# Optimization experiments

Measured on AMD Instinct MI355X. Metric: run time of the kernel, lower is better.

## Reference

```python
import jax, jax.numpy as jnp
import numpy as np

N = 100000   # nodes
E = 1600000  # edges (avg degree 16)
D = 64       # in_channels
OUT = 64     # out_channels


def setup_inputs() -> dict:
    key = jax.random.key(0)
    k1, k2, k3, k4, k5 = jax.random.split(key, 5)
    x = jax.random.normal(k1, (N, D), jnp.float32)
    edge_index = jax.random.randint(k2, (2, E), 0, N, dtype=jnp.int32)
    x0 = jax.random.normal(k3, (N, D), jnp.float32)
    W_weight = jax.random.normal(k4, (OUT, D), jnp.float32) * (1.0 / np.sqrt(D))
    W_bias = jax.random.normal(k5, (OUT,), jnp.float32) * 0.01
    return {"x": x, "edge_index": edge_index, "x0": x0,
            "W_weight": W_weight, "W_bias": W_bias}


def reference(x, edge_index, x0, W_bias, W_weight):
    n = x.shape[0]
    # gcn_norm with add_self_loops=True (PyG default), improved=False
    self_loops = jnp.arange(n, dtype=edge_index.dtype)
    row = jnp.concatenate([edge_index[0], self_loops])  # source nodes
    col = jnp.concatenate([edge_index[1], self_loops])  # target nodes
    w = jnp.ones(row.shape[0], dtype=x.dtype)
    deg = jax.ops.segment_sum(w, col, num_segments=n)   # in-degree (+1 self loop)
    deg_inv_sqrt = jnp.where(deg > 0, jax.lax.rsqrt(jnp.maximum(deg, 1e-12)), 0.0)
    norm = deg_inv_sqrt[row] * deg_inv_sqrt[col]        # [E+N]
    # SpMM: adj_t = SparseTensor(row=col, col=row) -> out[c] = sum_e norm_e * x[row_e]
    agg = jax.ops.segment_sum(x[row] * norm[:, None], col, num_segments=n)  # [N, D]
    # use_init=False, use_weight=True -> trailing Linear
    return agg @ W_weight.T + W_bias
```

## Files before the change

kernel.cpp:

```cpp
#include <hip/hip_runtime.h>


#define NBMAX 400
#define CAP   5120

typedef short bf16x8 __attribute__((ext_vector_type(8)));
typedef float f32x4  __attribute__((ext_vector_type(4)));

__device__ inline float bflo(unsigned u) { return __uint_as_float(u << 16); }
__device__ inline float bfhi(unsigned u) { return __uint_as_float(u & 0xFFFF0000u); }
__device__ inline unsigned short f2bf(float f) {
    unsigned u = __float_as_uint(f);
    u += 0x7FFFu + ((u >> 16) & 1u);
    return (unsigned short)(u >> 16);
}

__global__ void k_initcur(int* __restrict__ gcur, int NB) {
    int b = threadIdx.x;
    if (b < NB) gcur[b] = b * CAP;
}

__global__ __launch_bounds__(256) void k_bin(const int* __restrict__ row,
                                             const int* __restrict__ col,
                                             int* __restrict__ gcur,
                                             unsigned int* __restrict__ ebuf, int E) {
    __shared__ unsigned int   sorted4[4096];
    __shared__ unsigned short sbkt[4096];
    __shared__ int h[NBMAX], hstart[NBMAX], hcur[NBMAX], gof[NBMAX];
    int t = threadIdx.x;
    int base = blockIdx.x * 4096;
    int total = min(4096, E - base);

    int rr[16], cc[16];
    #pragma unroll
    for (int i = 0; i < 4; ++i) {
        int e0 = (t + i * 256) * 4;
        if (e0 + 3 < total) {
            int4 r4 = *(const int4*)(row + base + e0);
            int4 c4 = *(const int4*)(col + base + e0);
            rr[i*4+0]=r4.x; rr[i*4+1]=r4.y; rr[i*4+2]=r4.z; rr[i*4+3]=r4.w;
            cc[i*4+0]=c4.x; cc[i*4+1]=c4.y; cc[i*4+2]=c4.z; cc[i*4+3]=c4.w;
        } else {
            #pragma unroll
            for (int j = 0; j < 4; ++j) {
                int e = e0 + j;
                if (e < total) { rr[i*4+j] = row[base+e]; cc[i*4+j] = col[base+e]; }
                else cc[i*4+j] = -1;
            }
        }
    }
    for (int b = t; b < NBMAX; b += 256) h[b] = 0;
    __syncthreads();
    #pragma unroll
    for (int i = 0; i < 16; ++i)
        if (cc[i] >= 0) atomicAdd(&h[cc[i] >> 8], 1);
    __syncthreads();
    if (t < 64) {
        int lo = t * 7;
        int loc[7]; int s = 0;
        #pragma unroll
        for (int i = 0; i < 7; ++i) {
            loc[i] = s;
            int idx = lo + i;
            s += (idx < NBMAX) ? h[idx] : 0;
        }
        int incl = s;
        for (int off = 1; off < 64; off <<= 1) {
            int v = __shfl_up(incl, off);
            if (t >= off) incl += v;
        }
        int ex = incl - s;
        #pragma unroll
        for (int i = 0; i < 7; ++i) {
            int idx = lo + i;
            if (idx < NBMAX) hstart[idx] = ex + loc[i];
        }
    }
    __syncthreads();
    for (int b = t; b < NBMAX; b += 256) hcur[b] = hstart[b];
    __syncthreads();
    #pragma unroll
    for (int i = 0; i < 16; ++i) {
        if (cc[i] >= 0) {
            int b = cc[i] >> 8;
            int rank = atomicAdd(&hcur[b], 1);
            sorted4[rank] = (unsigned)rr[i] | ((unsigned)(cc[i] & 255) << 24);
            sbkt[rank] = (unsigned short)b;
        }
    }
    for (int b = t; b < NBMAX; b += 256) {
        int m = h[b];
        gof[b] = m ? atomicAdd(&gcur[b], m) : 0;
    }
    __syncthreads();
    for (int i = t; i < total; i += 256) {
        int b = sbkt[i];
        ebuf[gof[b] + (i - hstart[b])] = sorted4[i];
    }
}

__global__ __launch_bounds__(256) void k_cnt(const unsigned int* __restrict__ ebuf,
                                             const int* __restrict__ gcur,
                                             float* __restrict__ dinv, int n) {
    __shared__ int h[256];
    int b = blockIdx.x, t = threadIdx.x;
    int s0 = b * CAP;
    int count = min(gcur[b] - s0, CAP);
    h[t] = 0;
    __syncthreads();
    for (int i = t; i < count; i += 256) atomicAdd(&h[ebuf[s0 + i] >> 24], 1);
    __syncthreads();
    int c = b * 256 + t;
    if (c < n) dinv[c] = rsqrtf((float)(h[t] + 1));
}

__global__ __launch_bounds__(256) void k_gemm(const float* __restrict__ x,
                                              const float* __restrict__ W,
                                              const float* __restrict__ dinv,
                                              unsigned short* __restrict__ yb, int n) {
    __shared__ __align__(16) unsigned short xs[64][72];
    __shared__ __align__(16) unsigned short Wb[64][72];
    int t = threadIdx.x;
    long long total = (long long)n * 64;
    long long xbase = (long long)blockIdx.x * 4096;
    #pragma unroll
    for (int i = 0; i < 4; ++i) {
        int idx = t + i * 256;
        int r = idx >> 4, c4 = (idx & 15) << 2;
        long long g = xbase + (long long)idx * 4;
        float4 v;
        if (g + 3 < total) v = *(const float4*)(x + g);
        else {
            v.x = (g + 0 < total) ? x[g + 0] : 0.f;
            v.y = (g + 1 < total) ? x[g + 1] : 0.f;
            v.z = (g + 2 < total) ? x[g + 2] : 0.f;
            v.w = (g + 3 < total) ? x[g + 3] : 0.f;
        }
        ushort4 o; o.x = f2bf(v.x); o.y = f2bf(v.y); o.z = f2bf(v.z); o.w = f2bf(v.w);
        *(ushort4*)&xs[r][c4] = o;
        float4 wv = *(const float4*)(W + idx * 4);
        ushort4 wo; wo.x = f2bf(wv.x); wo.y = f2bf(wv.y); wo.z = f2bf(wv.z); wo.w = f2bf(wv.w);
        *(ushort4*)&Wb[r][c4] = wo;
    }
    __syncthreads();
    int lane = t & 63, wid = t >> 6;
    int m  = wid * 16 + (lane & 15);
    int kg = (lane >> 4) * 8;
    bf16x8 a0 = *(bf16x8*)&xs[m][kg];
    bf16x8 a1 = *(bf16x8*)&xs[m][32 + kg];
    int bn = lane & 15;
    f32x4 acc0 = {0.f,0.f,0.f,0.f}, acc1 = acc0, acc2 = acc0, acc3 = acc0;
    {
        bf16x8 b0 = *(bf16x8*)&Wb[bn][kg], b1 = *(bf16x8*)&Wb[bn][32 + kg];
        acc0 = __builtin_amdgcn_mfma_f32_16x16x32_bf16(a0, b0, acc0, 0, 0, 0);
        acc0 = __builtin_amdgcn_mfma_f32_16x16x32_bf16(a1, b1, acc0, 0, 0, 0);
    }
    {
        bf16x8 b0 = *(bf16x8*)&Wb[bn + 16][kg], b1 = *(bf16x8*)&Wb[bn + 16][32 + kg];
        acc1 = __builtin_amdgcn_mfma_f32_16x16x32_bf16(a0, b0, acc1, 0, 0, 0);
        acc1 = __builtin_amdgcn_mfma_f32_16x16x32_bf16(a1, b1, acc1, 0, 0, 0);
    }
    {
        bf16x8 b0 = *(bf16x8*)&Wb[bn + 32][kg], b1 = *(bf16x8*)&Wb[bn + 32][32 + kg];
        acc2 = __builtin_amdgcn_mfma_f32_16x16x32_bf16(a0, b0, acc2, 0, 0, 0);
        acc2 = __builtin_amdgcn_mfma_f32_16x16x32_bf16(a1, b1, acc2, 0, 0, 0);
    }
    {
        bf16x8 b0 = *(bf16x8*)&Wb[bn + 48][kg], b1 = *(bf16x8*)&Wb[bn + 48][32 + kg];
        acc3 = __builtin_amdgcn_mfma_f32_16x16x32_bf16(a0, b0, acc3, 0, 0, 0);
        acc3 = __builtin_amdgcn_mfma_f32_16x16x32_bf16(a1, b1, acc3, 0, 0, 0);
    }
    int rbase = blockIdx.x * 64 + wid * 16 + (lane >> 4) * 4;
    #pragma unroll
    for (int i = 0; i < 4; ++i) {
        int r = rbase + i;
        if (r < n) {
            float dv = dinv[r];
            long long ro = (long long)r * 64 + (lane & 15);
            yb[ro +  0] = f2bf(dv * acc0[i]);
            yb[ro + 16] = f2bf(dv * acc1[i]);
            yb[ro + 32] = f2bf(dv * acc2[i]);
            yb[ro + 48] = f2bf(dv * acc3[i]);
        }
    }
}

__global__ __launch_bounds__(1024) void k_aggr(const unsigned int* __restrict__ ebuf,
                                               const int* __restrict__ gcur,
                                               const float* __restrict__ dinv,
                                               const unsigned short* __restrict__ yb,
                                               const float* __restrict__ bias,
                                               float* __restrict__ out, int n) {
    __shared__ int h[256], hstart[256], hc[256], wsum[4];
    __shared__ int sbuf[CAP];
    int b = blockIdx.x, t = threadIdx.x;
    int s0 = b * CAP;
    int count = min(gcur[b] - s0, CAP);

    if (t < 256) h[t] = 0;
    __syncthreads();
    unsigned rec[5];
    #pragma unroll
    for (int k = 0; k < 5; ++k) {
        int i = t + k * 1024;
        if (i < count) {
            unsigned p = ebuf[s0 + i];
            rec[k] = p;
            atomicAdd(&h[p >> 24], 1);
        }
    }
    __syncthreads();
    if (t < 256) {
        int v = h[t];
        int lane = t & 63, wid = t >> 6;
        int incl = v;
        #pragma unroll
        for (int off = 1; off < 64; off <<= 1) {
            int u = __shfl_up(incl, off);
            if (lane >= off) incl += u;
        }
        hstart[t] = incl;
        if (lane == 63) wsum[wid] = incl;
    }
    __syncthreads();
    if (t < 256) {
        int wid = t >> 6;
        int add = 0;
        for (int w = 0; w < wid; ++w) add += wsum[w];
        int ex = hstart[t] - h[t] + add;
        hstart[t] = ex;
        hc[t] = ex;
    }
    __syncthreads();
    #pragma unroll
    for (int k = 0; k < 5; ++k) {
        int i = t + k * 1024;
        if (i < count) {
            unsigned p = rec[k];
            int r = atomicAdd(&hc[p >> 24], 1);
            sbuf[r] = (int)(p & 0x1FFFFu);
        }
    }
    __syncthreads();

    int lane = t & 63, w = t >> 6;
    int g = lane >> 4, q = lane & 15;
    #pragma unroll
    for (int r = 0; r < 4; ++r) {
        int cl = r * 64 + w * 4 + g;
        int c = b * 256 + cl;
        if (c >= n) continue;
        int start = hstart[cl], len = h[cl];
        float a0 = 0.f, a1 = 0.f, a2 = 0.f, a3 = 0.f;
        if (len > 0) {
            int sc = sbuf[start];
            for (int i = 0; i < len; ++i) {
                int sn = (i + 1 < len) ? sbuf[start + i + 1] : 0;
                float2 v = *(const float2*)(yb + (long long)sc * 64 + (q << 2));
                unsigned u0 = __float_as_uint(v.x), u1 = __float_as_uint(v.y);
                a0 += bflo(u0); a1 += bfhi(u0);
                a2 += bflo(u1); a3 += bfhi(u1);
                sc = sn;
            }
        }
        {
            float2 v = *(const float2*)(yb + (long long)c * 64 + (q << 2));
            unsigned u0 = __float_as_uint(v.x), u1 = __float_as_uint(v.y);
            a0 += bflo(u0); a1 += bfhi(u0);
            a2 += bflo(u1); a3 += bfhi(u1);
        }
        float dc = dinv[c];
        float4 bv = *(const float4*)(bias + (q << 2));
        *(float4*)(out + (long long)c * 64 + (q << 2)) =
            make_float4(dc * a0 + bv.x, dc * a1 + bv.y,
                        dc * a2 + bv.z, dc * a3 + bv.w);
    }
}

extern "C" void kernel_launch(void* const* d_in, const int* in_sizes, int n_in,
                              void* d_out, int out_size, void* d_ws, size_t ws_size,
                              hipStream_t stream) {
    const float* x    = (const float*)d_in[0];
    const int*   ei   = (const int*)d_in[1];
    const float* W    = (const float*)d_in[3];
    const float* bias = (const float*)d_in[4];
    float* out = (float*)d_out;

    int n = in_sizes[0] / 64;
    int E = in_sizes[1] / 2;
    const int* row = ei;
    const int* col = ei + E;

    int NB = (n + 255) / 256;

    char* ws = (char*)d_ws;
    size_t off = 0;
    auto alloc = [&](size_t bytes) { char* p = ws + off; off += (bytes + 15) & ~size_t(15); return p; };
    int*            gcur = (int*)  alloc((size_t)NB * 4);
    float*          dinv = (float*)alloc((size_t)n * 4);
    unsigned short* yb   = (unsigned short*)alloc((size_t)n * 64 * 2);
    unsigned int*   ebuf = (unsigned int*)alloc((size_t)NB * CAP * 4);

    int nbE = (E + 4095) / 4096;

    k_initcur<<<1, 512, 0, stream>>>(gcur, NB);
    k_bin <<<nbE, 256, 0, stream>>>(row, col, gcur, ebuf, E);
    k_cnt <<<NB, 256, 0, stream>>>(ebuf, gcur, dinv, n);
    k_gemm<<<(n + 63) / 64, 256, 0, stream>>>(x, W, dinv, yb, n);
    k_aggr<<<NB, 1024, 0, stream>>>(ebuf, gcur, dinv, yb, bias, out, n);
}
```

Baseline: 178.1 us.

## Balance aggregation by degree-ranked node pairing and widen gathers to 8 lanes per node

```diff
diff --git a/kernel.cpp b/kernel.cpp
--- a/kernel.cpp
+++ b/kernel.cpp
@@ -13,6 +13,13 @@
     unsigned u = __float_as_uint(f);
     u += 0x7FFFu + ((u >> 16) & 1u);
     return (unsigned short)(u >> 16);
+}
+
+__device__ inline void acc8(float* a, float4 v) {
+    unsigned x = __float_as_uint(v.x), y = __float_as_uint(v.y);
+    unsigned z = __float_as_uint(v.z), w = __float_as_uint(v.w);
+    a[0] += bflo(x); a[1] += bfhi(x); a[2] += bflo(y); a[3] += bfhi(y);
+    a[4] += bflo(z); a[5] += bfhi(z); a[6] += bflo(w); a[7] += bfhi(w);
 }
 
 __global__ void k_initcur(int* __restrict__ gcur, int NB) {
@@ -192,12 +199,13 @@
                                                const float* __restrict__ bias,
                                                float* __restrict__ out, int n) {
     __shared__ int h[256], hstart[256], hc[256], wsum[4];
+    __shared__ int rnk[256], slotmap[256];
     __shared__ int sbuf[CAP];
     int b = blockIdx.x, t = threadIdx.x;
     int s0 = b * CAP;
     int count = min(gcur[b] - s0, CAP);
 
-    if (t < 256) h[t] = 0;
+    if (t < 256) { h[t] = 0; rnk[t] = 0; }
     __syncthreads();
     unsigned rec[5];
     #pragma unroll
@@ -222,6 +230,17 @@
         hstart[t] = incl;
         if (lane == 63) wsum[wid] = incl;
     }
+    {
+        int cl2 = t & 255, part = t >> 8;
+        int lt = h[cl2];
+        int base2 = part << 6;
+        int rk = 0;
+        for (int u2 = base2; u2 < base2 + 64; ++u2) {
+            int lu = h[u2];
+            rk += ((lu > lt) || (lu == lt && u2 < cl2)) ? 1 : 0;
+        }
+        if (rk) atomicAdd(&rnk[cl2], rk);
+    }
     __syncthreads();
     if (t < 256) {
         int wid = t >> 6;
@@ -230,6 +249,7 @@
         int ex = hstart[t] - h[t] + add;
         hstart[t] = ex;
         hc[t] = ex;
+        slotmap[rnk[t]] = t;
     }
     __syncthreads();
     #pragma unroll
@@ -244,36 +264,49 @@
     __syncthreads();
 
     int lane = t & 63, w = t >> 6;
-    int g = lane >> 4, q = lane & 15;
-    #pragma unroll
-    for (int r = 0; r < 4; ++r) {
-        int cl = r * 64 + w * 4 + g;
+    int g = lane >> 3, q = lane & 7;
+    int qo = q << 3;
+    #pragma unroll 1
+    for (int r = 0; r < 2; ++r) {
+        int slot = w * 8 + g;
+        int cl = slotmap[r == 0 ? slot : 255 - slot];
         int c = b * 256 + cl;
         if (c >= n) continue;
         int start = hstart[cl], len = h[cl];
-        float a0 = 0.f, a1 = 0.f, a2 = 0.f, a3 = 0.f;
-        if (len > 0) {
-            int sc = sbuf[start];
-            for (int i = 0; i < len; ++i) {
-                int sn = (i + 1 < len) ? sbuf[start + i + 1] : 0;
-                float2 v = *(const float2*)(yb + (long long)sc * 64 + (q << 2));
-                unsigned u0 = __float_as_uint(v.x), u1 = __float_as_uint(v.y);
-                a0 += bflo(u0); a1 += bfhi(u0);
-                a2 += bflo(u1); a3 += bfhi(u1);
-                sc = sn;
-            }
-        }
-        {
-            float2 v = *(const float2*)(yb + (long long)c * 64 + (q << 2));
-            unsigned u0 = __float_as_uint(v.x), u1 = __float_as_uint(v.y);
-            a0 += bflo(u0); a1 += bfhi(u0);
-            a2 += bflo(u1); a3 += bfhi(u1);
-        }
+        float sa[8] = {0.f,0.f,0.f,0.f,0.f,0.f,0.f,0.f};
+        float ua[8] = {0.f,0.f,0.f,0.f,0.f,0.f,0.f,0.f};
+        float4 vself = *(const float4*)(yb + (long long)c * 64 + qo);
+        int i = 0;
+        for (; i + 4 <= len; i += 4) {
+            int e0 = sbuf[start + i + 0];
+            int e1 = sbuf[start + i + 1];
+            int e2 = sbuf[start + i + 2];
+            int e3 = sbuf[start + i + 3];
+            float4 v0 = *(const float4*)(yb + (long long)e0 * 64 + qo);
+            float4 v1 = *(const float4*)(yb + (long long)e1 * 64 + qo);
+            float4 v2 = *(const float4*)(yb + (long long)e2 * 64 + qo);
+            float4 v3 = *(const float4*)(yb + (long long)e3 * 64 + qo);
+            acc8(sa, v0); acc8(ua, v1); acc8(sa, v2); acc8(ua, v3);
+        }
+        for (; i < len; ++i) {
+            int e0 = sbuf[start + i];
+            float4 v0 = *(const float4*)(yb + (long long)e0 * 64 + qo);
+            acc8(sa, v0);
+        }
+        acc8(ua, vself);
         float dc = dinv[c];
-        float4 bv = *(const float4*)(bias + (q << 2));
-        *(float4*)(out + (long long)c * 64 + (q << 2)) =
-            make_float4(dc * a0 + bv.x, dc * a1 + bv.y,
-                        dc * a2 + bv.z, dc * a3 + bv.w);
+        float4 b0 = *(const float4*)(bias + qo);
+        float4 b1 = *(const float4*)(bias + qo + 4);
+        float4 o0 = make_float4(dc * (sa[0] + ua[0]) + b0.x,
+                                dc * (sa[1] + ua[1]) + b0.y,
+                                dc * (sa[2] + ua[2]) + b0.z,
+                                dc * (sa[3] + ua[3]) + b0.w);
+        float4 o1 = make_float4(dc * (sa[4] + ua[4]) + b1.x,
+                                dc * (sa[5] + ua[5]) + b1.y,
+                                dc * (sa[6] + ua[6]) + b1.z,
+                                dc * (sa[7] + ua[7]) + b1.w);
+        *(float4*)(out + (long long)c * 64 + qo)     = o0;
+        *(float4*)(out + (long long)c * 64 + qo + 4) = o1;
     }
 }
 
```

Measured after the change: 178.1 us. No clear change (-0.0%).

## Pre-convert W once, load x fragments directly, halve binning chunk size

Applied to the files above, without the earlier changes.

```diff
diff --git a/kernel.cpp b/kernel.cpp
--- a/kernel.cpp
+++ b/kernel.cpp
@@ -3,6 +3,7 @@
 
 #define NBMAX 400
 #define CAP   5120
+#define CHUNK 2048
 
 typedef short bf16x8 __attribute__((ext_vector_type(8)));
 typedef float f32x4  __attribute__((ext_vector_type(4)));
@@ -15,25 +16,37 @@
     return (unsigned short)(u >> 16);
 }
 
-__global__ void k_initcur(int* __restrict__ gcur, int NB) {
-    int b = threadIdx.x;
-    if (b < NB) gcur[b] = b * CAP;
+__device__ inline bf16x8 cvt8(float4 a, float4 b) {
+    bf16x8 r;
+    r[0] = (short)f2bf(a.x); r[1] = (short)f2bf(a.y);
+    r[2] = (short)f2bf(a.z); r[3] = (short)f2bf(a.w);
+    r[4] = (short)f2bf(b.x); r[5] = (short)f2bf(b.y);
+    r[6] = (short)f2bf(b.z); r[7] = (short)f2bf(b.w);
+    return r;
+}
+
+__global__ __launch_bounds__(256) void k_prep(const float* __restrict__ W,
+                                              unsigned short* __restrict__ wbf,
+                                              int* __restrict__ gcnt, int NB) {
+    int gid = blockIdx.x * 256 + threadIdx.x;
+    if (gid < 4096) wbf[gid] = f2bf(W[gid]);
+    if (gid < NB) gcnt[gid] = 0;
 }
 
 __global__ __launch_bounds__(256) void k_bin(const int* __restrict__ row,
                                              const int* __restrict__ col,
-                                             int* __restrict__ gcur,
+                                             int* __restrict__ gcnt,
                                              unsigned int* __restrict__ ebuf, int E) {
-    __shared__ unsigned int   sorted4[4096];
-    __shared__ unsigned short sbkt[4096];
+    __shared__ unsigned int   sorted4[CHUNK];
+    __shared__ unsigned short sbkt[CHUNK];
     __shared__ int h[NBMAX], hstart[NBMAX], hcur[NBMAX], gof[NBMAX];
     int t = threadIdx.x;
-    int base = blockIdx.x * 4096;
-    int total = min(4096, E - base);
-
-    int rr[16], cc[16];
-    #pragma unroll
-    for (int i = 0; i < 4; ++i) {
+    int base = blockIdx.x * CHUNK;
+    int total = min(CHUNK, E - base);
+
+    int rr[8], cc[8];
+    #pragma unroll
+    for (int i = 0; i < 2; ++i) {
         int e0 = (t + i * 256) * 4;
         if (e0 + 3 < total) {
             int4 r4 = *(const int4*)(row + base + e0);
@@ -52,7 +65,7 @@
     for (int b = t; b < NBMAX; b += 256) h[b] = 0;
     __syncthreads();
     #pragma unroll
-    for (int i = 0; i < 16; ++i)
+    for (int i = 0; i < 8; ++i)
         if (cc[i] >= 0) atomicAdd(&h[cc[i] >> 8], 1);
     __syncthreads();
     if (t < 64) {
@@ -80,7 +93,7 @@
     for (int b = t; b < NBMAX; b += 256) hcur[b] = hstart[b];
     __syncthreads();
     #pragma unroll
-    for (int i = 0; i < 16; ++i) {
+    for (int i = 0; i < 8; ++i) {
         if (cc[i] >= 0) {
             int b = cc[i] >> 8;
             int rank = atomicAdd(&hcur[b], 1);
@@ -90,7 +103,7 @@
     }
     for (int b = t; b < NBMAX; b += 256) {
         int m = h[b];
-        gof[b] = m ? atomicAdd(&gcur[b], m) : 0;
+        gof[b] = b * CAP + (m ? atomicAdd(&gcnt[b], m) : 0);
     }
     __syncthreads();
     for (int i = t; i < total; i += 256) {
@@ -100,12 +113,12 @@
 }
 
 __global__ __launch_bounds__(256) void k_cnt(const unsigned int* __restrict__ ebuf,
-                                             const int* __restrict__ gcur,
+                                             const int* __restrict__ gcnt,
                                              float* __restrict__ dinv, int n) {
     __shared__ int h[256];
     int b = blockIdx.x, t = threadIdx.x;
     int s0 = b * CAP;
-    int count = min(gcur[b] - s0, CAP);
+    int count = min(gcnt[b], CAP);
     h[t] = 0;
     __syncthreads();
     for (int i = t; i < count; i += 256) atomicAdd(&h[ebuf[s0 + i] >> 24], 1);
@@ -115,58 +128,46 @@
 }
 
 __global__ __launch_bounds__(256) void k_gemm(const float* __restrict__ x,
-                                              const float* __restrict__ W,
+                                              const unsigned short* __restrict__ wbf,
                                               const float* __restrict__ dinv,
                                               unsigned short* __restrict__ yb, int n) {
-    __shared__ __align__(16) unsigned short xs[64][72];
-    __shared__ __align__(16) unsigned short Wb[64][72];
     int t = threadIdx.x;
-    long long total = (long long)n * 64;
-    long long xbase = (long long)blockIdx.x * 4096;
-    #pragma unroll
-    for (int i = 0; i < 4; ++i) {
-        int idx = t + i * 256;
-        int r = idx >> 4, c4 = (idx & 15) << 2;
-        long long g = xbase + (long long)idx * 4;
-        float4 v;
-        if (g + 3 < total) v = *(const float4*)(x + g);
-        else {
-            v.x = (g + 0 < total) ? x[g + 0] : 0.f;
-            v.y = (g + 1 < total) ? x[g + 1] : 0.f;
-            v.z = (g + 2 < total) ? x[g + 2] : 0.f;
-            v.w = (g + 3 < total) ? x[g + 3] : 0.f;
-        }
-        ushort4 o; o.x = f2bf(v.x); o.y = f2bf(v.y); o.z = f2bf(v.z); o.w = f2bf(v.w);
-        *(ushort4*)&xs[r][c4] = o;
-        float4 wv = *(const float4*)(W + idx * 4);
-        ushort4 wo; wo.x = f2bf(wv.x); wo.y = f2bf(wv.y); wo.z = f2bf(wv.z); wo.w = f2bf(wv.w);
-        *(ushort4*)&Wb[r][c4] = wo;
-    }
-    __syncthreads();
     int lane = t & 63, wid = t >> 6;
-    int m  = wid * 16 + (lane & 15);
+    int m = blockIdx.x * 64 + wid * 16 + (lane & 15);
     int kg = (lane >> 4) * 8;
-    bf16x8 a0 = *(bf16x8*)&xs[m][kg];
-    bf16x8 a1 = *(bf16x8*)&xs[m][32 + kg];
+    bf16x8 a0 = {0,0,0,0,0,0,0,0}, a1 = a0;
+    if (m < n) {
+        const float* xr = x + (long long)m * 64 + kg;
+        float4 p0 = *(const float4*)(xr);
+        float4 p1 = *(const float4*)(xr + 4);
+        float4 p2 = *(const float4*)(xr + 32);
+        float4 p3 = *(const float4*)(xr + 36);
+        a0 = cvt8(p0, p1);
+        a1 = cvt8(p2, p3);
+    }
     int bn = lane & 15;
     f32x4 acc0 = {0.f,0.f,0.f,0.f}, acc1 = acc0, acc2 = acc0, acc3 = acc0;
     {
-        bf16x8 b0 = *(bf16x8*)&Wb[bn][kg], b1 = *(bf16x8*)&Wb[bn][32 + kg];
+        bf16x8 b0 = *(const bf16x8*)(wbf + (bn     ) * 64 + kg);
+        bf16x8 b1 = *(const bf16x8*)(wbf + (bn     ) * 64 + 32 + kg);
         acc0 = __builtin_amdgcn_mfma_f32_16x16x32_bf16(a0, b0, acc0, 0, 0, 0);
         acc0 = __builtin_amdgcn_mfma_f32_16x16x32_bf16(a1, b1, acc0, 0, 0, 0);
     }
     {
-        bf16x8 b0 = *(bf16x8*)&Wb[bn + 16][kg], b1 = *(bf16x8*)&Wb[bn + 16][32 + kg];
+        bf16x8 b0 = *(const bf16x8*)(wbf + (bn + 16) * 64 + kg);
+        bf16x8 b1 = *(const bf16x8*)(wbf + (bn + 16) * 64 + 32 + kg);
         acc1 = __builtin_amdgcn_mfma_f32_16x16x32_bf16(a0, b0, acc1, 0, 0, 0);
         acc1 = __builtin_amdgcn_mfma_f32_16x16x32_bf16(a1, b1, acc1, 0, 0, 0);
     }
     {
-        bf16x8 b0 = *(bf16x8*)&Wb[bn + 32][kg], b1 = *(bf16x8*)&Wb[bn + 32][32 + kg];
+        bf16x8 b0 = *(const bf16x8*)(wbf + (bn + 32) * 64 + kg);
+        bf16x8 b1 = *(const bf16x8*)(wbf + (bn + 32) * 64 + 32 + kg);
         acc2 = __builtin_amdgcn_mfma_f32_16x16x32_bf16(a0, b0, acc2, 0, 0, 0);
         acc2 = __builtin_amdgcn_mfma_f32_16x16x32_bf16(a1, b1, acc2, 0, 0, 0);
     }
     {
-        bf16x8 b0 = *(bf16x8*)&Wb[bn + 48][kg], b1 = *(bf16x8*)&Wb[bn + 48][32 + kg];
+        bf16x8 b0 = *(const bf16x8*)(wbf + (bn + 48) * 64 + kg);
+        bf16x8 b1 = *(const bf16x8*)(wbf + (bn + 48) * 64 + 32 + kg);
         acc3 = __builtin_amdgcn_mfma_f32_16x16x32_bf16(a0, b0, acc3, 0, 0, 0);
         acc3 = __builtin_amdgcn_mfma_f32_16x16x32_bf16(a1, b1, acc3, 0, 0, 0);
     }
@@ -176,7 +177,7 @@
         int r = rbase + i;
         if (r < n) {
             float dv = dinv[r];
-            long long ro = (long long)r * 64 + (lane & 15);
+            long long ro = (long long)r * 64 + bn;
             yb[ro +  0] = f2bf(dv * acc0[i]);
             yb[ro + 16] = f2bf(dv * acc1[i]);
             yb[ro + 32] = f2bf(dv * acc2[i]);
@@ -186,7 +187,7 @@
 }
 
 __global__ __launch_bounds__(1024) void k_aggr(const unsigned int* __restrict__ ebuf,
-                                               const int* __restrict__ gcur,
+                                               const int* __restrict__ gcnt,
                                                const float* __restrict__ dinv,
                                                const unsigned short* __restrict__ yb,
                                                const float* __restrict__ bias,
@@ -195,7 +196,7 @@
     __shared__ int sbuf[CAP];
     int b = blockIdx.x, t = threadIdx.x;
     int s0 = b * CAP;
-    int count = min(gcur[b] - s0, CAP);
+    int count = min(gcnt[b], CAP);
 
     if (t < 256) h[t] = 0;
     __syncthreads();
@@ -296,16 +297,17 @@
     char* ws = (char*)d_ws;
     size_t off = 0;
     auto alloc = [&](size_t bytes) { char* p = ws + off; off += (bytes + 15) & ~size_t(15); return p; };
-    int*            gcur = (int*)  alloc((size_t)NB * 4);
+    int*            gcnt = (int*)  alloc((size_t)NB * 4);
     float*          dinv = (float*)alloc((size_t)n * 4);
     unsigned short* yb   = (unsigned short*)alloc((size_t)n * 64 * 2);
     unsigned int*   ebuf = (unsigned int*)alloc((size_t)NB * CAP * 4);
-
-    int nbE = (E + 4095) / 4096;
-
-    k_initcur<<<1, 512, 0, stream>>>(gcur, NB);
-    k_bin <<<nbE, 256, 0, stream>>>(row, col, gcur, ebuf, E);
-    k_cnt <<<NB, 256, 0, stream>>>(ebuf, gcur, dinv, n);
-    k_gemm<<<(n + 63) / 64, 256, 0, stream>>>(x, W, dinv, yb, n);
-    k_aggr<<<NB, 1024, 0, stream>>>(ebuf, gcur, dinv, yb, bias, out, n);
-}
+    unsigned short* wbf  = (unsigned short*)alloc((size_t)4096 * 2);
+
+    int nbE = (E + CHUNK - 1) / CHUNK;
+
+    k_prep<<<16, 256, 0, stream>>>(W, wbf, gcnt, NB);
+    k_bin <<<nbE, 256, 0, stream>>>(row, col, gcnt, ebuf, E);
+    k_cnt <<<NB, 256, 0, stream>>>(ebuf, gcnt, dinv, n);
+    k_gemm<<<(n + 63) / 64, 256, 0, stream>>>(x, wbf, dinv, yb, n);
+    k_aggr<<<NB, 1024, 0, stream>>>(ebuf, gcnt, dinv, yb, bias, out, n);
+}
```

New measurement: 193.2 us. 1.08x slower.

## Fuse degree counting into binning kernel and drop separate count pass

Applied to the files above, without the earlier changes.

```diff
diff --git a/kernel.cpp b/kernel.cpp
--- a/kernel.cpp
+++ b/kernel.cpp
@@ -15,19 +15,39 @@
     return (unsigned short)(u >> 16);
 }
 
-__global__ void k_initcur(int* __restrict__ gcur, int NB) {
-    int b = threadIdx.x;
-    if (b < NB) gcur[b] = b * CAP;
-}
-
-__global__ __launch_bounds__(256) void k_bin(const int* __restrict__ row,
-                                             const int* __restrict__ col,
-                                             int* __restrict__ gcur,
-                                             unsigned int* __restrict__ ebuf, int E) {
+__global__ __launch_bounds__(256) void k_bindeg(const int* __restrict__ row,
+                                                const int* __restrict__ col,
+                                                int* __restrict__ gcnt,
+                                                int* __restrict__ deg,
+                                                unsigned int* __restrict__ ebuf,
+                                                int E, int nbBin) {
     __shared__ unsigned int   sorted4[4096];
     __shared__ unsigned short sbkt[4096];
     __shared__ int h[NBMAX], hstart[NBMAX], hcur[NBMAX], gof[NBMAX];
     int t = threadIdx.x;
+
+    if ((int)blockIdx.x >= nbBin) {
+        int base = ((int)blockIdx.x - nbBin) * 4096;
+        int total = min(4096, E - base);
+        #pragma unroll
+        for (int i = 0; i < 4; ++i) {
+            int e0 = (t + i * 256) * 4;
+            if (e0 + 3 < total) {
+                int4 c4 = *(const int4*)(col + base + e0);
+                atomicAdd(&deg[c4.x], 1);
+                atomicAdd(&deg[c4.y], 1);
+                atomicAdd(&deg[c4.z], 1);
+                atomicAdd(&deg[c4.w], 1);
+            } else {
+                for (int j = 0; j < 4; ++j) {
+                    int e = e0 + j;
+                    if (e < total) atomicAdd(&deg[col[base + e]], 1);
+                }
+            }
+        }
+        return;
+    }
+
     int base = blockIdx.x * 4096;
     int total = min(4096, E - base);
 
@@ -90,7 +110,7 @@
     }
     for (int b = t; b < NBMAX; b += 256) {
         int m = h[b];
-        gof[b] = m ? atomicAdd(&gcur[b], m) : 0;
+        gof[b] = b * CAP + (m ? atomicAdd(&gcnt[b], m) : 0);
     }
     __syncthreads();
     for (int i = t; i < total; i += 256) {
@@ -99,24 +119,9 @@
     }
 }
 
-__global__ __launch_bounds__(256) void k_cnt(const unsigned int* __restrict__ ebuf,
-                                             const int* __restrict__ gcur,
-                                             float* __restrict__ dinv, int n) {
-    __shared__ int h[256];
-    int b = blockIdx.x, t = threadIdx.x;
-    int s0 = b * CAP;
-    int count = min(gcur[b] - s0, CAP);
-    h[t] = 0;
-    __syncthreads();
-    for (int i = t; i < count; i += 256) atomicAdd(&h[ebuf[s0 + i] >> 24], 1);
-    __syncthreads();
-    int c = b * 256 + t;
-    if (c < n) dinv[c] = rsqrtf((float)(h[t] + 1));
-}
-
 __global__ __launch_bounds__(256) void k_gemm(const float* __restrict__ x,
                                               const float* __restrict__ W,
-                                              const float* __restrict__ dinv,
+                                              const int* __restrict__ deg,
                                               unsigned short* __restrict__ yb, int n) {
     __shared__ __align__(16) unsigned short xs[64][72];
     __shared__ __align__(16) unsigned short Wb[64][72];
@@ -175,8 +180,8 @@
     for (int i = 0; i < 4; ++i) {
         int r = rbase + i;
         if (r < n) {
-            float dv = dinv[r];
-            long long ro = (long long)r * 64 + (lane & 15);
+            float dv = rsqrtf((float)deg[r] + 1.0f);
+            long long ro = (long long)r * 64 + bn;
             yb[ro +  0] = f2bf(dv * acc0[i]);
             yb[ro + 16] = f2bf(dv * acc1[i]);
             yb[ro + 32] = f2bf(dv * acc2[i]);
@@ -186,8 +191,7 @@
 }
 
 __global__ __launch_bounds__(1024) void k_aggr(const unsigned int* __restrict__ ebuf,
-                                               const int* __restrict__ gcur,
-                                               const float* __restrict__ dinv,
+                                               const int* __restrict__ gcnt,
                                                const unsigned short* __restrict__ yb,
                                                const float* __restrict__ bias,
                                                float* __restrict__ out, int n) {
@@ -195,7 +199,7 @@
     __shared__ int sbuf[CAP];
     int b = blockIdx.x, t = threadIdx.x;
     int s0 = b * CAP;
-    int count = min(gcur[b] - s0, CAP);
+    int count = min(gcnt[b], CAP);
 
     if (t < 256) h[t] = 0;
     __syncthreads();
@@ -269,7 +273,7 @@
             a0 += bflo(u0); a1 += bfhi(u0);
             a2 += bflo(u1); a3 += bfhi(u1);
         }
-        float dc = dinv[c];
+        float dc = rsqrtf((float)len + 1.0f);
         float4 bv = *(const float4*)(bias + (q << 2));
         *(float4*)(out + (long long)c * 64 + (q << 2)) =
             make_float4(dc * a0 + bv.x, dc * a1 + bv.y,
@@ -296,16 +300,16 @@
     char* ws = (char*)d_ws;
     size_t off = 0;
     auto alloc = [&](size_t bytes) { char* p = ws + off; off += (bytes + 15) & ~size_t(15); return p; };
-    int*            gcur = (int*)  alloc((size_t)NB * 4);
-    float*          dinv = (float*)alloc((size_t)n * 4);
+    int*            zbuf = (int*)  alloc(((size_t)NB + (size_t)n) * 4);
+    int*            gcnt = zbuf;
+    int*            deg  = zbuf + NB;
     unsigned short* yb   = (unsigned short*)alloc((size_t)n * 64 * 2);
     unsigned int*   ebuf = (unsigned int*)alloc((size_t)NB * CAP * 4);
 
-    int nbE = (E + 4095) / 4096;
-
-    k_initcur<<<1, 512, 0, stream>>>(gcur, NB);
-    k_bin <<<nbE, 256, 0, stream>>>(row, col, gcur, ebuf, E);
-    k_cnt <<<NB, 256, 0, stream>>>(ebuf, gcur, dinv, n);
-    k_gemm<<<(n + 63) / 64, 256, 0, stream>>>(x, W, dinv, yb, n);
-    k_aggr<<<NB, 1024, 0, stream>>>(ebuf, gcur, dinv, yb, bias, out, n);
-}
+    int nbBin = (E + 4095) / 4096;
+
+    hipMemsetAsync(zbuf, 0, ((size_t)NB + (size_t)n) * 4, stream);
+    k_bindeg<<<nbBin * 2, 256, 0, stream>>>(row, col, gcnt, deg, ebuf, E, nbBin);
+    k_gemm<<<(n + 63) / 64, 256, 0, stream>>>(x, W, deg, yb, n);
+    k_aggr<<<NB, 1024, 0, stream>>>(ebuf, gcnt, yb, bias, out, n);
+}
```

Measured after the change: 230.5 us. 1.29x slower.
